# Kernel optimization log

Hardware: AMD Instinct MI355X
Metric: run time of the kernel (lower is better)

## Reference

```python
import jax, jax.numpy as jnp
import numpy as np

N_NODES = 100000
N_EDGES = 800000
F_IN = 16
F_OUT = 16
NB = 4          # basis terms per coordinate dimension (dims=[4,4] -> K=16)
OUTPUT_SCALING = 1.0 / 128.0


def hat_basis(u, n):
    """'linear' RBF: hat functions on [-1,1]. u: [E] -> [E, n]."""
    centers = jnp.linspace(-1.0, 1.0, n, dtype=u.dtype)   # [n]
    width = 2.0 / (n - 1)
    return jnp.maximum(0.0, 1.0 - jnp.abs(u[:, None] - centers[None, :]) / width)


def setup_inputs() -> dict:
    key = jax.random.key(0)
    k1, k2, k3, k4, k5 = jax.random.split(key, 5)
    x = jax.random.normal(k1, (N_NODES, F_IN), dtype=jnp.float32)
    edge_attr = jax.random.normal(k2, (N_EDGES, 2), dtype=jnp.float32) * 0.7
    # conv weight tensor: [K, F_in, F_out], xavier-ish scale with gain 1/sqrt(34)
    W = jax.random.normal(k3, (NB * NB, F_IN, F_OUT), dtype=jnp.float32) * (
        (1.0 / np.sqrt(34.0)) * np.sqrt(2.0 / (F_IN + F_OUT)))
    edge_index_i = jax.random.randint(k4, (N_EDGES,), 0, N_NODES, dtype=jnp.int64)
    edge_index_j = jax.random.randint(k5, (N_EDGES,), 0, N_NODES, dtype=jnp.int64)
    return {"x": x, "edge_attr": edge_attr, "W": W,
            "edge_index_i": edge_index_i, "edge_index_j": edge_index_j}


def reference(x, edge_attr, W, edge_index_i, edge_index_j):
    # --- process(): centerIgnore mask, clamp, cartesian mapping (identity) ---
    mask = edge_index_i != edge_index_j                      # [E]
    mapped = jnp.clip(edge_attr, -1.0, 1.0)                  # [E, 2]

    # --- tensor-product 'linear' basis evaluation: [E, K] ---
    bx = hat_basis(mapped[:, 0], NB)                         # [E, NB]
    by = hat_basis(mapped[:, 1], NB)                         # [E, NB]
    basis = (bx[:, :, None] * by[:, None, :]).reshape(mapped.shape[0], NB * NB)

    # --- continuous conv: gather, per-edge basis-weighted linear, scatter ---
    xj = x[edge_index_j]                                     # [E, F_in] gather
    u = jnp.einsum('ei,kio->eko', xj, W)                     # [E, K, F_out]
    msg = jnp.einsum('ek,eko->eo', basis, u)                 # [E, F_out]
    msg = jnp.where(mask[:, None], msg, jnp.zeros((), msg.dtype))
    out = jax.ops.segment_sum(msg, edge_index_i, num_segments=x.shape[0])
    return out * OUTPUT_SCALING
```

## Files before the change

### kernel.cpp

```cpp
#include <hip/hip_runtime.h>

#define N_NODES 100000
#define N_EDGES 800000
#define NBY    ((N_NODES + 255) / 256)
#define HBLK   ((N_EDGES + 255) / 256)
#define OVF_CAP 65536
#define GA     250
#define CHUNK  3200
#define NBINS  512
#define NPB    196
#define CAPB   2048
#define GB_T   1024
#define CURSTRIDE 64

__device__ __forceinline__ unsigned short f2bf(float f) {
    union { float f; unsigned u; } v; v.f = f;
    unsigned u = v.u;
    return (unsigned short)((u + 0x7FFFu + ((u >> 16) & 1u)) >> 16);
}
__device__ __forceinline__ float bflo(unsigned u) {
    union { unsigned u; float f; } v; v.u = u << 16; return v.f;
}
__device__ __forceinline__ float bfhi(unsigned u) {
    union { unsigned u; float f; } v; v.u = u & 0xFFFF0000u; return v.f;
}

__global__ __launch_bounds__(256) void bucket_build(
    const float* __restrict__ edge_attr,
    const int* __restrict__ ei, const int* __restrict__ ej,
    int* __restrict__ cursor, uint2* __restrict__ bkt,
    int* __restrict__ ovfCnt, int* __restrict__ ovf) {
    const int b = blockIdx.x;
    __shared__ int hist[NBINS];
    __shared__ unsigned rawA[CHUNK];
    __shared__ unsigned rawB[CHUNK];
    __shared__ short rawBin[CHUNK];
    const int tid = threadIdx.x;
    for (int k = tid; k < NBINS; k += 256) hist[k] = 0;
    __syncthreads();
    const int base = b * CHUNK;

    for (int i = 0; i < CHUNK; i += 256) {
        const int j = i + tid;
        if (j >= CHUNK) continue;
        const int e = base + j;
        short binS = -1;
        if (e < N_EDGES) {
            const int di = ei[e];
            const int sj = ej[e];
            if (di != sj) {
                const float2 ea = ((const float2*)edge_attr)[e];
                float ux = fminf(fmaxf(ea.x, -1.f), 1.f);
                float uy = fminf(fmaxf(ea.y, -1.f), 1.f);
                float tx = (ux + 1.f) * 1.5f;
                float ty = (uy + 1.f) * 1.5f;
                int kx0 = min((int)tx, 2);
                int ky0 = min((int)ty, 2);
                float fx = tx - (float)kx0;
                float fy = ty - (float)ky0;
                unsigned fx12 = (unsigned)(fx * 4095.f + 0.5f);
                unsigned fy12 = (unsigned)(fy * 4095.f + 0.5f);
                const int bin = di / NPB;
                const unsigned local = (unsigned)(di - bin * NPB);
                rawA[j] = (unsigned)(sj * 512 + (kx0 * 4 + ky0) * 32);
                rawB[j] = fx12 | (fy12 << 12) | (local << 24);
                binS = (short)bin;
                atomicAdd(&hist[bin], 1);
            }
        }
        rawBin[j] = binS;
    }
    __syncthreads();

    for (int k = tid; k < NBINS; k += 256) {
        const int c = hist[k];
        int g = 0;
        if (c > 0) g = atomicAdd(&cursor[k * CURSTRIDE], c);
        hist[k] = k * CAPB + g;
    }
    __syncthreads();

    for (int i = 0; i < CHUNK; i += 256) {
        const int j = i + tid;
        if (j >= CHUNK) continue;
        const int bin = rawBin[j];
        if (bin < 0) continue;
        const int s = atomicAdd(&hist[bin], 1);
        if (s - bin * CAPB < CAPB) {
            bkt[s] = make_uint2(rawA[j], rawB[j]);
        } else {
            const int o = atomicAdd(ovfCnt, 1);
            if (o < OVF_CAP) ovf[o] = base + j;
        }
    }
}

__global__ __launch_bounds__(GB_T) void gather_conv(
    const int* __restrict__ cursor, const uint2* __restrict__ bkt,
    const float* __restrict__ x, const float* __restrict__ W,
    float* __restrict__ out,
    const int* __restrict__ ovfCnt, const int* __restrict__ ovf,
    const float* __restrict__ edge_attr, const int* __restrict__ ei,
    const int* __restrict__ ej) {
    const int bin = blockIdx.x;
    const int tid = threadIdx.x;
    __shared__ uint2 sorted[CAPB];
    __shared__ __align__(16) char u_buf[20480];
    __shared__ int h[NPB];
    __shared__ int st[NPB], en[NPB], cur[NPB];
    __shared__ int wsum[4];
    __shared__ float tile[NPB * 16];
    uint2* raw = (uint2*)u_buf;
    float* Wl  = (float*)u_buf;

    for (int j = tid; j < NPB; j += GB_T) h[j] = 0;
    __syncthreads();

    const int cnt = min(cursor[bin * CURSTRIDE], CAPB);
    const int pad = (cnt + NPB <= CAPB) ? 1 : 0;
    const uint2* rb = bkt + (size_t)bin * CAPB;

    for (int p = tid; p < cnt; p += GB_T) {
        uint2 r = rb[p];
        raw[p] = r;
        atomicAdd(&h[r.y >> 24], 1);
    }
    __syncthreads();

    const int lane = tid & 63;
    const int wid  = tid >> 6;
    int c0 = 0, v = 0;
    if (tid < 256) {
        c0 = (tid < NPB) ? h[tid] : 0;
        v = c0;
#pragma unroll
        for (int off = 1; off < 64; off <<= 1) {
            int u = __shfl_up(v, off);
            if (lane >= off) v += u;
        }
        if (lane == 63) wsum[wid] = v;
    }
    __syncthreads();
    if (tid < NPB) {
        int pfx = 0;
#pragma unroll
        for (int w = 0; w < 4; ++w)
            if (w < wid) pfx += wsum[w];
        const int incl = v + pfx;
        const int sh = tid * pad;
        en[tid]  = incl + sh;
        st[tid]  = incl - c0 + sh;
        cur[tid] = incl - c0 + sh;
    }
    __syncthreads();

    for (int p = tid; p < cnt; p += GB_T) {
        uint2 r = raw[p];
        int pos = atomicAdd(&cur[r.y >> 24], 1);
        sorted[pos] = r;
    }
    __syncthreads();

    {
        float4 w = ((const float4*)W)[tid];
        const int k = tid >> 6, i = (tid >> 2) & 15, o4 = tid & 3;
        *(float4*)&Wl[k * 320 + i * 20 + o4 * 4] = w;
    }
    __syncthreads();

    const float U = 1.f / 4095.f;
    const float S = 1.f / 128.f;
    if (tid < 4 * NPB) {
        const int node = tid >> 2;
        const int q4 = tid & 3;
        float t[16][4];
#pragma unroll
        for (int k = 0; k < 16; ++k)
#pragma unroll
            for (int i = 0; i < 4; ++i) t[k][i] = 0.f;

        const int lo = st[node], hi2 = en[node];
        uint2 m = make_uint2(0u, 0u);
        float4 xv = make_float4(0.f, 0.f, 0.f, 0.f);
        if (lo < hi2) {
            m = sorted[lo];
            xv = ((const float4*)x)[(m.x >> 9) * 4 + q4];
        }
        for (int idx = lo; idx < hi2; ++idx) {
            const uint2 mc = m;
            const float4 xc = xv;
            if (idx + 1 < hi2) {
                m = sorted[idx + 1];
                xv = ((const float4*)x)[(m.x >> 9) * 4 + q4];
            }
            const unsigned koff = (mc.x >> 5) & 15u;
            const int kx0 = (int)(koff >> 2);
            const int ky0 = (int)(koff & 3u);
            const float fx = (float)(mc.y & 0xFFFu) * U;
            const float fy = (float)((mc.y >> 12) & 0xFFFu) * U;
            float wx[4], wy[4];
#pragma unroll
            for (int a = 0; a < 4; ++a) {
                wx[a] = (a == kx0) ? (1.f - fx) : ((a == kx0 + 1) ? fx : 0.f);
                wy[a] = (a == ky0) ? (1.f - fy) : ((a == ky0 + 1) ? fy : 0.f);
            }
            const float xr[4] = {xc.x, xc.y, xc.z, xc.w};
#pragma unroll
            for (int kx = 0; kx < 4; ++kx)
#pragma unroll
                for (int ky = 0; ky < 4; ++ky) {
                    const float w = wx[kx] * wy[ky];
#pragma unroll
                    for (int i = 0; i < 4; ++i)
                        t[kx * 4 + ky][i] = fmaf(w, xr[i], t[kx * 4 + ky][i]);
                }
        }

        float po[16];
#pragma unroll
        for (int o = 0; o < 16; ++o) po[o] = 0.f;
#pragma unroll
        for (int k = 0; k < 16; ++k)
#pragma unroll
            for (int il = 0; il < 4; ++il) {
                const float tv = t[k][il];
                const float4* wr = (const float4*)&Wl[k * 320 + (q4 * 4 + il) * 20];
                const float4 w0 = wr[0], w1 = wr[1], w2 = wr[2], w3 = wr[3];
                po[0]  = fmaf(tv, w0.x, po[0]);  po[1]  = fmaf(tv, w0.y, po[1]);
                po[2]  = fmaf(tv, w0.z, po[2]);  po[3]  = fmaf(tv, w0.w, po[3]);
                po[4]  = fmaf(tv, w1.x, po[4]);  po[5]  = fmaf(tv, w1.y, po[5]);
                po[6]  = fmaf(tv, w1.z, po[6]);  po[7]  = fmaf(tv, w1.w, po[7]);
                po[8]  = fmaf(tv, w2.x, po[8]);  po[9]  = fmaf(tv, w2.y, po[9]);
                po[10] = fmaf(tv, w2.z, po[10]); po[11] = fmaf(tv, w2.w, po[11]);
                po[12] = fmaf(tv, w3.x, po[12]); po[13] = fmaf(tv, w3.y, po[13]);
                po[14] = fmaf(tv, w3.z, po[14]); po[15] = fmaf(tv, w3.w, po[15]);
            }

#pragma unroll
        for (int o = 0; o < 16; ++o) {
            po[o] += __shfl_xor(po[o], 1);
            po[o] += __shfl_xor(po[o], 2);
        }
        if (q4 == 0) {
            float* tr = &tile[node * 16];
#pragma unroll
            for (int o = 0; o < 16; ++o) tr[o] = po[o] * S;
        }
    }
    __syncthreads();

    const int m = min(*ovfCnt, OVF_CAP);
    if (m > 0) {
        const int nlo = bin * NPB;
        const int nhi = min(nlo + NPB, N_NODES);
        for (int i = tid; i < m; i += GB_T) {
            const int e = ovf[i];
            const int di = ei[e];
            if (di < nlo || di >= nhi) continue;
            const int sj = ej[e];
            const float2 ea = ((const float2*)edge_attr)[e];
            float ux = fminf(fmaxf(ea.x, -1.f), 1.f);
            float uy = fminf(fmaxf(ea.y, -1.f), 1.f);
            float tx = (ux + 1.f) * 1.5f, ty = (uy + 1.f) * 1.5f;
            int kx0 = min((int)tx, 2), ky0 = min((int)ty, 2);
            float fx = tx - (float)kx0, fy = ty - (float)ky0;
            float wgt[4] = {(1.f-fx)*(1.f-fy)*S, (1.f-fx)*fy*S, fx*(1.f-fy)*S, fx*fy*S};
            int kidx[4] = {kx0*4+ky0, kx0*4+ky0+1, (kx0+1)*4+ky0, (kx0+1)*4+ky0+1};
            const float* xj = x + (size_t)sj * 16;
            float msg[16];
#pragma unroll
            for (int o = 0; o < 16; ++o) msg[o] = 0.f;
#pragma unroll
            for (int p = 0; p < 4; ++p) {
                const float* wk = Wl + kidx[p] * 320;
                for (int ii = 0; ii < 16; ++ii) {
                    float xw = xj[ii] * wgt[p];
#pragma unroll
                    for (int o = 0; o < 16; ++o)
                        msg[o] = fmaf(xw, wk[ii * 20 + o], msg[o]);
                }
            }
            float* tr = &tile[(di - nlo) * 16];
#pragma unroll
            for (int o = 0; o < 16; ++o) atomicAdd(tr + o, msg[o]);
        }
        __syncthreads();
    }

    const int base = bin * NPB * 16;
    const int lim = N_NODES * 16 - base;
    for (int j = tid; j < NPB * 16; j += GB_T)
        if (j < lim) out[base + j] = tile[j];
}

__global__ __launch_bounds__(256) void y_only_kernel(
    const float* __restrict__ x, const float* __restrict__ W,
    unsigned short* __restrict__ Y) {
    const int n = blockIdx.x * 256 + threadIdx.x;
    const int kbase = blockIdx.y * 4;
    if (n >= N_NODES) return;
    const float4* xv = (const float4*)(x + n * 16);
    float4 a = xv[0], b = xv[1], c = xv[2], d = xv[3];
    float xr[16] = {a.x,a.y,a.z,a.w, b.x,b.y,b.z,b.w,
                    c.x,c.y,c.z,c.w, d.x,d.y,d.z,d.w};
    float acc[4][16];
#pragma unroll
    for (int kk = 0; kk < 4; ++kk)
#pragma unroll
        for (int o = 0; o < 16; ++o) acc[kk][o] = 0.f;
#pragma unroll
    for (int i = 0; i < 16; ++i)
#pragma unroll
        for (int kk = 0; kk < 4; ++kk) {
            const float* wrow = W + ((kbase + kk) * 256 + i * 16);
#pragma unroll
            for (int o = 0; o < 16; ++o)
                acc[kk][o] = fmaf(xr[i], wrow[o], acc[kk][o]);
        }
    unsigned short* dst = Y + (size_t)n * 256 + kbase * 16;
#pragma unroll
    for (int kk = 0; kk < 4; ++kk) {
        unsigned pk[8];
#pragma unroll
        for (int q = 0; q < 8; ++q)
            pk[q] = (unsigned)f2bf(acc[kk][2*q]) | ((unsigned)f2bf(acc[kk][2*q+1]) << 16);
        uint4* p = (uint4*)(dst + kk * 16);
        p[0] = make_uint4(pk[0], pk[1], pk[2], pk[3]);
        p[1] = make_uint4(pk[4], pk[5], pk[6], pk[7]);
    }
}

__global__ __launch_bounds__(256) void edge_kernel(
    const float* __restrict__ edge_attr, const int* __restrict__ ei,
    const int* __restrict__ ej, const unsigned short* __restrict__ Y,
    float* __restrict__ out) {
    const int e = blockIdx.x * 256 + threadIdx.x;
    if (e >= N_EDGES) return;
    const int di = ei[e];
    const int sj = ej[e];
    const float2 ea = ((const float2*)edge_attr)[e];
    if (di == sj) return;
    float ux = fminf(fmaxf(ea.x, -1.f), 1.f);
    float uy = fminf(fmaxf(ea.y, -1.f), 1.f);
    float tx = (ux + 1.f) * 1.5f;
    float ty = (uy + 1.f) * 1.5f;
    int kx0 = min((int)tx, 2);
    int ky0 = min((int)ty, 2);
    float fx = tx - (float)kx0;
    float fy = ty - (float)ky0;
    const float S = 1.f / 128.f;
    float w00 = (1.f - fx) * (1.f - fy) * S;
    float w01 = (1.f - fx) * fy * S;
    float w10 = fx * (1.f - fy) * S;
    float w11 = fx * fy * S;
    const unsigned short* base = Y + (size_t)sj * 256 + (kx0 * 4 + ky0) * 16;
    const uint4* pA = (const uint4*)base;
    const uint4* pB = (const uint4*)(base + 64);
    uint4 a0 = pA[0], a1 = pA[1], a2 = pA[2], a3 = pA[3];
    uint4 b0 = pB[0], b1 = pB[1], b2 = pB[2], b3 = pB[3];
    unsigned ra0[8] = {a0.x,a0.y,a0.z,a0.w, a1.x,a1.y,a1.z,a1.w};
    unsigned ra1[8] = {a2.x,a2.y,a2.z,a2.w, a3.x,a3.y,a3.z,a3.w};
    unsigned rb0[8] = {b0.x,b0.y,b0.z,b0.w, b1.x,b1.y,b1.z,b1.w};
    unsigned rb1[8] = {b2.x,b2.y,b2.z,b2.w, b3.x,b3.y,b3.z,b3.w};
    float* o16 = out + (size_t)di * 16;
#pragma unroll
    for (int q = 0; q < 8; ++q) {
        float m0 = bflo(ra0[q]) * w00 + bflo(ra1[q]) * w01
                 + bflo(rb0[q]) * w10 + bflo(rb1[q]) * w11;
        float m1 = bfhi(ra0[q]) * w00 + bfhi(ra1[q]) * w01
                 + bfhi(rb0[q]) * w10 + bfhi(rb1[q]) * w11;
        atomicAdd(o16 + 2 * q, m0);
        atomicAdd(o16 + 2 * q + 1, m1);
    }
}

__global__ __launch_bounds__(256) void edge_direct(
    const float* __restrict__ x, const float* __restrict__ edge_attr,
    const float* __restrict__ W, const int* __restrict__ ei,
    const int* __restrict__ ej, float* __restrict__ out) {
    const int e = blockIdx.x * 256 + threadIdx.x;
    if (e >= N_EDGES) return;
    const int di = ei[e];
    const int sj = ej[e];
    const float2 ea = ((const float2*)edge_attr)[e];
    if (di == sj) return;
    float ux = fminf(fmaxf(ea.x, -1.f), 1.f);
    float uy = fminf(fmaxf(ea.y, -1.f), 1.f);
    float tx = (ux + 1.f) * 1.5f, ty = (uy + 1.f) * 1.5f;
    int kx0 = min((int)tx, 2), ky0 = min((int)ty, 2);
    float fx = tx - (float)kx0, fy = ty - (float)ky0;
    const float S = 1.f / 128.f;
    float wgt[4] = {(1.f-fx)*(1.f-fy)*S, (1.f-fx)*fy*S, fx*(1.f-fy)*S, fx*fy*S};
    int kidx[4] = {kx0*4+ky0, kx0*4+ky0+1, (kx0+1)*4+ky0, (kx0+1)*4+ky0+1};
    const float* xj = x + (size_t)sj * 16;
    float xr[16];
#pragma unroll
    for (int i = 0; i < 16; ++i) xr[i] = xj[i];
    float msg[16];
#pragma unroll
    for (int o = 0; o < 16; ++o) msg[o] = 0.f;
#pragma unroll
    for (int p = 0; p < 4; ++p) {
        const float* wk = W + kidx[p] * 256;
#pragma unroll
        for (int i = 0; i < 16; ++i) {
            float xw = xr[i] * wgt[p];
#pragma unroll
            for (int o = 0; o < 16; ++o)
                msg[o] = fmaf(xw, wk[i * 16 + o], msg[o]);
        }
    }
    float* o16 = out + (size_t)di * 16;
#pragma unroll
    for (int o = 0; o < 16; ++o) atomicAdd(o16 + o, msg[o]);
}

extern "C" void kernel_launch(void* const* d_in, const int* in_sizes, int n_in,
                              void* d_out, int out_size, void* d_ws, size_t ws_size,
                              hipStream_t stream) {
    const float* x         = (const float*)d_in[0];
    const float* edge_attr = (const float*)d_in[1];
    const float* W         = (const float*)d_in[2];
    const int*   ei        = (const int*)d_in[3];
    const int*   ej        = (const int*)d_in[4];
    float* out = (float*)d_out;
    char* ws = (char*)d_ws;

    const size_t oCur    = 0;
    const size_t oOvfCnt = oCur + (size_t)NBINS * CURSTRIDE * 4;
    const size_t oOvf    = oOvfCnt + 16;
    const size_t oBkt    = oOvf + (size_t)OVF_CAP * 4;
    const size_t total   = oBkt + (size_t)NBINS * CAPB * 8;

    if (ws_size >= total) {
        int*   cursor = (int*)(ws + oCur);
        int*   ovfCnt = (int*)(ws + oOvfCnt);
        int*   ovf    = (int*)(ws + oOvf);
        uint2* bkt    = (uint2*)(ws + oBkt);

        hipMemsetAsync(cursor, 0, (size_t)NBINS * CURSTRIDE * 4 + 16, stream);
        bucket_build<<<GA, 256, 0, stream>>>(
            edge_attr, ei, ej, cursor, bkt, ovfCnt, ovf);
        gather_conv<<<NBINS, GB_T, 0, stream>>>(
            cursor, bkt, x, W, out, ovfCnt, ovf, edge_attr, ei, ej);
        return;
    }

    const size_t yBytes = (size_t)N_NODES * 512;
    if (ws_size >= yBytes) {
        hipMemsetAsync(d_out, 0, (size_t)out_size * sizeof(float), stream);
        unsigned short* Y = (unsigned short*)d_ws;
        dim3 gA(NBY, 4);
        y_only_kernel<<<gA, 256, 0, stream>>>(x, W, Y);
        edge_kernel<<<HBLK, 256, 0, stream>>>(edge_attr, ei, ej, Y, out);
    } else {
        hipMemsetAsync(d_out, 0, (size_t)out_size * sizeof(float), stream);
        edge_direct<<<HBLK, 256, 0, stream>>>(x, edge_attr, W, ei, ej, out);
    }
}
```

Baseline: 130.3 us.

## Fuse memset, bucket build and gather-conv into one cooperative kernel

Replaces the memset plus two-kernel pipeline with a single cooperative launch of 512 blocks of 1024 threads. Grid-wide syncs separate the phases: cursor reset and histogramming, bucket scatter, and per-bin sort plus convolution. This removes launch gaps and the separate memset, and keeps raw per-chunk data in shared memory across the grid barrier. In exchange it adds grid-sync cost, fixes the bucket-build phase at 256 blocks, and relies on all 512 blocks being co-resident, falling back to the old path if the cooperative launch fails.

```diff
diff --git a/kernel.cpp b/kernel.cpp
--- a/kernel.cpp
+++ b/kernel.cpp
@@ -1,4 +1,7 @@
 #include <hip/hip_runtime.h>
+#include <hip/hip_cooperative_groups.h>
+
+namespace cg = cooperative_groups;
 
 #define N_NODES 100000
 #define N_EDGES 800000
@@ -12,6 +15,10 @@
 #define CAPB   2048
 #define GB_T   1024
 #define CURSTRIDE 64
+#define FB     512
+#define FT     1024
+#define PAB    256
+#define PACHUNK 3125
 
 __device__ __forceinline__ unsigned short f2bf(float f) {
     union { float f; unsigned u; } v; v.f = f;
@@ -23,6 +30,277 @@
 }
 __device__ __forceinline__ float bfhi(unsigned u) {
     union { unsigned u; float f; } v; v.u = u & 0xFFFF0000u; return v.f;
+}
+
+__global__ __launch_bounds__(FT, 8) void fused_all(
+    int* __restrict__ cursor, uint2* __restrict__ bkt,
+    const float* __restrict__ x, const float* __restrict__ W,
+    float* __restrict__ out, int* __restrict__ ovfCnt, int* __restrict__ ovf,
+    const float* __restrict__ edge_attr, const int* __restrict__ ei,
+    const int* __restrict__ ej) {
+    cg::grid_group grid = cg::this_grid();
+    const int b = blockIdx.x;
+    const int tid = threadIdx.x;
+
+    __shared__ __align__(16) char SM[52576];
+    uint2* sorted = (uint2*)SM;
+    uint2* rawS   = (uint2*)(SM + 16384);
+    float* Wl     = (float*)(SM + 16384);
+    float* tile   = (float*)(SM + 36864);
+    int*   h      = (int*)(SM + 49408);
+    int*   st     = (int*)(SM + 50192);
+    int*   en     = (int*)(SM + 50976);
+    int*   cur    = (int*)(SM + 51760);
+    int*   wsum   = (int*)(SM + 52544);
+    unsigned* rawA = (unsigned*)SM;
+    unsigned* rawB = (unsigned*)(SM + 12512);
+    short*  rawBin = (short*)(SM + 25024);
+    int*    hist   = (int*)(SM + 31280);
+
+    if (tid == 0) {
+        atomicExch(&cursor[b * CURSTRIDE], 0);
+        if (b == 0) atomicExch(ovfCnt, 0);
+    }
+    for (int j = tid; j < NPB; j += FT) h[j] = 0;
+
+    if (b < PAB) {
+        if (tid < NBINS) hist[tid] = 0;
+        __syncthreads();
+        const int base = b * PACHUNK;
+        for (int i = 0; i < PACHUNK; i += FT) {
+            const int j = i + tid;
+            if (j >= PACHUNK) continue;
+            const int e = base + j;
+            short binS = -1;
+            const int di = ei[e];
+            const int sj = ej[e];
+            if (di != sj) {
+                const float2 ea = ((const float2*)edge_attr)[e];
+                float ux = fminf(fmaxf(ea.x, -1.f), 1.f);
+                float uy = fminf(fmaxf(ea.y, -1.f), 1.f);
+                float tx = (ux + 1.f) * 1.5f;
+                float ty = (uy + 1.f) * 1.5f;
+                int kx0 = min((int)tx, 2);
+                int ky0 = min((int)ty, 2);
+                float fx = tx - (float)kx0;
+                float fy = ty - (float)ky0;
+                unsigned fx12 = (unsigned)(fx * 4095.f + 0.5f);
+                unsigned fy12 = (unsigned)(fy * 4095.f + 0.5f);
+                const int bn = di / NPB;
+                const unsigned local = (unsigned)(di - bn * NPB);
+                rawA[j] = (unsigned)(sj * 512 + (kx0 * 4 + ky0) * 32);
+                rawB[j] = fx12 | (fy12 << 12) | (local << 24);
+                binS = (short)bn;
+                atomicAdd(&hist[bn], 1);
+            }
+            rawBin[j] = binS;
+        }
+    }
+
+    grid.sync();
+
+    if (b < PAB) {
+        if (tid < NBINS) {
+            const int c = hist[tid];
+            int g = 0;
+            if (c > 0) g = atomicAdd(&cursor[tid * CURSTRIDE], c);
+            hist[tid] = tid * CAPB + g;
+        }
+        __syncthreads();
+        const int base = b * PACHUNK;
+        for (int i = 0; i < PACHUNK; i += FT) {
+            const int j = i + tid;
+            if (j >= PACHUNK) continue;
+            const int bn = rawBin[j];
+            if (bn < 0) continue;
+            const int s = atomicAdd(&hist[bn], 1);
+            if (s - bn * CAPB < CAPB) {
+                bkt[s] = make_uint2(rawA[j], rawB[j]);
+            } else {
+                const int o = atomicAdd(ovfCnt, 1);
+                if (o < OVF_CAP) ovf[o] = base + j;
+            }
+        }
+    }
+
+    grid.sync();
+
+    const int bin = b;
+    const int cnt = min(cursor[bin * CURSTRIDE], CAPB);
+    const int pad = (cnt + NPB <= CAPB) ? 1 : 0;
+    const uint2* rb = bkt + (size_t)bin * CAPB;
+
+    for (int p = tid; p < cnt; p += FT) {
+        uint2 r = rb[p];
+        rawS[p] = r;
+        atomicAdd(&h[r.y >> 24], 1);
+    }
+    __syncthreads();
+
+    const int lane = tid & 63;
+    const int wid  = tid >> 6;
+    int c0 = 0, v = 0;
+    if (tid < 256) {
+        c0 = (tid < NPB) ? h[tid] : 0;
+        v = c0;
+#pragma unroll
+        for (int off = 1; off < 64; off <<= 1) {
+            int u = __shfl_up(v, off);
+            if (lane >= off) v += u;
+        }
+        if (lane == 63) wsum[wid] = v;
+    }
+    __syncthreads();
+    if (tid < NPB) {
+        int pfx = 0;
+#pragma unroll
+        for (int w = 0; w < 4; ++w)
+            if (w < wid) pfx += wsum[w];
+        const int incl = v + pfx;
+        const int sh = tid * pad;
+        en[tid]  = incl + sh;
+        st[tid]  = incl - c0 + sh;
+        cur[tid] = incl - c0 + sh;
+    }
+    __syncthreads();
+
+    for (int p = tid; p < cnt; p += FT) {
+        uint2 r = rawS[p];
+        int pos = atomicAdd(&cur[r.y >> 24], 1);
+        sorted[pos] = r;
+    }
+    __syncthreads();
+
+    {
+        float4 w = ((const float4*)W)[tid];
+        const int k = tid >> 6, i2 = (tid >> 2) & 15, o4 = tid & 3;
+        *(float4*)&Wl[k * 320 + i2 * 20 + o4 * 4] = w;
+    }
+    __syncthreads();
+
+    const float U = 1.f / 4095.f;
+    const float S = 1.f / 128.f;
+    if (tid < 4 * NPB) {
+        const int node = tid >> 2;
+        const int q4 = tid & 3;
+        float t[16][4];
+#pragma unroll
+        for (int k = 0; k < 16; ++k)
+#pragma unroll
+            for (int i = 0; i < 4; ++i) t[k][i] = 0.f;
+
+        const int lo = st[node], hi2 = en[node];
+        uint2 m = make_uint2(0u, 0u);
+        float4 xv = make_float4(0.f, 0.f, 0.f, 0.f);
+        if (lo < hi2) {
+            m = sorted[lo];
+            xv = ((const float4*)x)[(m.x >> 9) * 4 + q4];
+        }
+        for (int idx = lo; idx < hi2; ++idx) {
+            const uint2 mc = m;
+            const float4 xc = xv;
+            if (idx + 1 < hi2) {
+                m = sorted[idx + 1];
+                xv = ((const float4*)x)[(m.x >> 9) * 4 + q4];
+            }
+            const unsigned koff = (mc.x >> 5) & 15u;
+            const int kx0 = (int)(koff >> 2);
+            const int ky0 = (int)(koff & 3u);
+            const float fx = (float)(mc.y & 0xFFFu) * U;
+            const float fy = (float)((mc.y >> 12) & 0xFFFu) * U;
+            float wx[4], wy[4];
+#pragma unroll
+            for (int a = 0; a < 4; ++a) {
+                wx[a] = (a == kx0) ? (1.f - fx) : ((a == kx0 + 1) ? fx : 0.f);
+                wy[a] = (a == ky0) ? (1.f - fy) : ((a == ky0 + 1) ? fy : 0.f);
+            }
+            const float xr[4] = {xc.x, xc.y, xc.z, xc.w};
+#pragma unroll
+            for (int kx = 0; kx < 4; ++kx)
+#pragma unroll
+                for (int ky = 0; ky < 4; ++ky) {
+                    const float w = wx[kx] * wy[ky];
+#pragma unroll
+                    for (int i = 0; i < 4; ++i)
+                        t[kx * 4 + ky][i] = fmaf(w, xr[i], t[kx * 4 + ky][i]);
+                }
+        }
+
+        float po[16];
+#pragma unroll
+        for (int o = 0; o < 16; ++o) po[o] = 0.f;
+#pragma unroll
+        for (int k = 0; k < 16; ++k)
+#pragma unroll
+            for (int il = 0; il < 4; ++il) {
+                const float tv = t[k][il];
+                const float4* wr = (const float4*)&Wl[k * 320 + (q4 * 4 + il) * 20];
+                const float4 w0 = wr[0], w1 = wr[1], w2 = wr[2], w3 = wr[3];
+                po[0]  = fmaf(tv, w0.x, po[0]);  po[1]  = fmaf(tv, w0.y, po[1]);
+                po[2]  = fmaf(tv, w0.z, po[2]);  po[3]  = fmaf(tv, w0.w, po[3]);
+                po[4]  = fmaf(tv, w1.x, po[4]);  po[5]  = fmaf(tv, w1.y, po[5]);
+                po[6]  = fmaf(tv, w1.z, po[6]);  po[7]  = fmaf(tv, w1.w, po[7]);
+                po[8]  = fmaf(tv, w2.x, po[8]);  po[9]  = fmaf(tv, w2.y, po[9]);
+                po[10] = fmaf(tv, w2.z, po[10]); po[11] = fmaf(tv, w2.w, po[11]);
+                po[12] = fmaf(tv, w3.x, po[12]); po[13] = fmaf(tv, w3.y, po[13]);
+                po[14] = fmaf(tv, w3.z, po[14]); po[15] = fmaf(tv, w3.w, po[15]);
+            }
+
+#pragma unroll
+        for (int o = 0; o < 16; ++o) {
+            po[o] += __shfl_xor(po[o], 1);
+            po[o] += __shfl_xor(po[o], 2);
+        }
+        if (q4 == 0) {
+            float* tr = &tile[node * 16];
+#pragma unroll
+            for (int o = 0; o < 16; ++o) tr[o] = po[o] * S;
+        }
+    }
+    __syncthreads();
+
+    const int mv = min(*ovfCnt, OVF_CAP);
+    if (mv > 0) {
+        const int nlo = bin * NPB;
+        const int nhi = min(nlo + NPB, N_NODES);
+        for (int i = tid; i < mv; i += FT) {
+            const int e = ovf[i];
+            const int di = ei[e];
+            if (di < nlo || di >= nhi) continue;
+            const int sj = ej[e];
+            const float2 ea = ((const float2*)edge_attr)[e];
+            float ux = fminf(fmaxf(ea.x, -1.f), 1.f);
+            float uy = fminf(fmaxf(ea.y, -1.f), 1.f);
+            float tx = (ux + 1.f) * 1.5f, ty = (uy + 1.f) * 1.5f;
+            int kx0 = min((int)tx, 2), ky0 = min((int)ty, 2);
+            float fx = tx - (float)kx0, fy = ty - (float)ky0;
+            float wgt[4] = {(1.f-fx)*(1.f-fy)*S, (1.f-fx)*fy*S, fx*(1.f-fy)*S, fx*fy*S};
+            int kidx[4] = {kx0*4+ky0, kx0*4+ky0+1, (kx0+1)*4+ky0, (kx0+1)*4+ky0+1};
+            const float* xj = x + (size_t)sj * 16;
+            float msg[16];
+#pragma unroll
+            for (int o = 0; o < 16; ++o) msg[o] = 0.f;
+#pragma unroll
+            for (int p = 0; p < 4; ++p) {
+                const float* wk = Wl + kidx[p] * 320;
+                for (int ii = 0; ii < 16; ++ii) {
+                    float xw = xj[ii] * wgt[p];
+#pragma unroll
+                    for (int o = 0; o < 16; ++o)
+                        msg[o] = fmaf(xw, wk[ii * 20 + o], msg[o]);
+                }
+            }
+            float* tr = &tile[(di - nlo) * 16];
+#pragma unroll
+            for (int o = 0; o < 16; ++o) atomicAdd(tr + o, msg[o]);
+        }
+        __syncthreads();
+    }
+
+    const int base2 = bin * NPB * 16;
+    const int lim = N_NODES * 16 - base2;
+    for (int j = tid; j < NPB * 16; j += FT)
+        if (j < lim) out[base2 + j] = tile[j];
 }
 
 __global__ __launch_bounds__(256) void bucket_build(
@@ -39,7 +317,6 @@
     for (int k = tid; k < NBINS; k += 256) hist[k] = 0;
     __syncthreads();
     const int base = b * CHUNK;
-
     for (int i = 0; i < CHUNK; i += 256) {
         const int j = i + tid;
         if (j >= CHUNK) continue;
@@ -71,7 +348,6 @@
         rawBin[j] = binS;
     }
     __syncthreads();
-
     for (int k = tid; k < NBINS; k += 256) {
         const int c = hist[k];
         int g = 0;
@@ -79,7 +355,6 @@
         hist[k] = k * CAPB + g;
     }
     __syncthreads();
-
     for (int i = 0; i < CHUNK; i += 256) {
         const int j = i + tid;
         if (j >= CHUNK) continue;
@@ -438,6 +713,14 @@
         int*   ovf    = (int*)(ws + oOvf);
         uint2* bkt    = (uint2*)(ws + oBkt);
 
+        void* params[] = {(void*)&cursor, (void*)&bkt, (void*)&x, (void*)&W,
+                          (void*)&out, (void*)&ovfCnt, (void*)&ovf,
+                          (void*)&edge_attr, (void*)&ei, (void*)&ej};
+        hipError_t err = hipLaunchCooperativeKernel(
+            fused_all, dim3(FB), dim3(FT), params, 0, stream);
+        if (err == hipSuccess) return;
+        (void)hipGetLastError();
+
         hipMemsetAsync(cursor, 0, (size_t)NBINS * CURSTRIDE * 4 + 16, stream);
         bucket_build<<<GA, 256, 0, stream>>>(
             edge_attr, ei, ej, cursor, bkt, ovfCnt, ovf);
```

New measurement: 400.1 us. 3.07x slower.
